# Optimization experiments

Measured on AMD Instinct MI355X. Metric: run time of the kernel, lower is better.

## Reference

```python
import jax, jax.numpy as jnp
import numpy as np

N_HEAD = 8
HEAD_DIM = 32  # 256 / 8
MASK_VALUE = -10000.0

def setup_inputs() -> dict:
    key = jax.random.key(0)
    k1, k2, k3 = jax.random.split(key, 3)
    B, S, D = 8, 2048, 256
    x = jax.random.normal(k1, (B, S, D), dtype=jnp.float32)
    # kaiming_normal fan_in-based std ~ sqrt(2/fan_in)
    w_qkv = jax.random.normal(k2, (3 * D, D), dtype=jnp.float32) * np.sqrt(2.0 / D)
    b_qkv = jnp.zeros((3 * D,), dtype=jnp.float32)
    w_out = jax.random.normal(k3, (D, D), dtype=jnp.float32) * np.sqrt(2.0 / D)
    b_out = jnp.zeros((D,), dtype=jnp.float32)
    return {"x": x, "w_qkv": w_qkv, "b_qkv": b_qkv, "w_out": w_out, "b_out": b_out}

def reference(x, w_qkv, b_qkv, w_out, b_out):
    B, S, D = x.shape
    qkv = x @ w_qkv.T + b_qkv                      # [B,S,3D]
    q, k, v = jnp.split(qkv, 3, axis=-1)           # each [B,S,D]
    def split_heads(t):
        return t.reshape(B, S, N_HEAD, HEAD_DIM).transpose(0, 2, 1, 3)  # [B,H,S,hd]
    q, k, v = split_heads(q), split_heads(k), split_heads(v)
    scores = jnp.einsum('bhqd,bhkd->bhqk', q, k) / jnp.sqrt(jnp.float32(HEAD_DIM))
    causal = jnp.tril(jnp.ones((S, S), dtype=bool))
    scores = jnp.where(causal[None, None], scores, jnp.float32(MASK_VALUE))
    attn = jax.nn.softmax(scores, axis=-1)          # dropout p=0 (eval)
    out = jnp.einsum('bhqk,bhkd->bhqd', attn, v)    # [B,H,S,hd]
    out = out.transpose(0, 2, 1, 3).reshape(B, S, D)  # merge heads
    out = out @ w_out.T + b_out
    return (out, attn)
```

## Files before the change

kernel.cpp:

```cpp
#include <hip/hip_runtime.h>
#include <cmath>

#define NB 8
#define NS 2048
#define ND 256
#define NH 8
#define HD 32
#define NM (NB*NS)
#define QS_LOG2 (0.17677669529663689f * 1.4426950408889634f)
#define OUT_ATTN ((size_t)NM * ND)

typedef __attribute__((ext_vector_type(8))) short bf16x8;
typedef __attribute__((ext_vector_type(4))) float f32x4;

__device__ __forceinline__ ushort f2b(float f) {
  union { float f; uint32_t u; } v; v.f = f;
  const uint32_t r = (v.u + 0x7FFFu + ((v.u >> 16) & 1u)) >> 16;
  return (ushort)r;
}
__device__ __forceinline__ float b2f(ushort u) {
  union { uint32_t u; float f; } v; v.u = ((uint32_t)u) << 16;
  return v.f;
}

__global__ __launch_bounds__(256) void prep_kernel(
    const float* __restrict__ x, const float* __restrict__ wq,
    const float* __restrict__ wo,
    ushort* __restrict__ xh, ushort* __restrict__ xl,
    ushort* __restrict__ wqh, ushort* __restrict__ wql,
    ushort* __restrict__ woh) {
  const int g = blockIdx.x * 256 + threadIdx.x;
  if (g < 1048576) {
    const float4 v = ((const float4*)x)[g];
    ushort4 h, l;
    h.x = f2b(v.x); l.x = f2b(v.x - b2f(h.x));
    h.y = f2b(v.y); l.y = f2b(v.y - b2f(h.y));
    h.z = f2b(v.z); l.z = f2b(v.z - b2f(h.z));
    h.w = f2b(v.w); l.w = f2b(v.w - b2f(h.w));
    ((ushort4*)xh)[g] = h; ((ushort4*)xl)[g] = l;
  } else if (g < 1048576 + 49152) {
    const int t = g - 1048576;
    const float4 v = ((const float4*)wq)[t];
    ushort4 h, l;
    h.x = f2b(v.x); l.x = f2b(v.x - b2f(h.x));
    h.y = f2b(v.y); l.y = f2b(v.y - b2f(h.y));
    h.z = f2b(v.z); l.z = f2b(v.z - b2f(h.z));
    h.w = f2b(v.w); l.w = f2b(v.w - b2f(h.w));
    ((ushort4*)wqh)[t] = h; ((ushort4*)wql)[t] = l;
  } else if (g < 1048576 + 49152 + 16384) {
    const int t = g - (1048576 + 49152);
    const float4 v = ((const float4*)wo)[t];
    ushort4 h;
    h.x = f2b(v.x); h.y = f2b(v.y); h.z = f2b(v.z); h.w = f2b(v.w);
    ((ushort4*)woh)[t] = h;
  }
}

__global__ __launch_bounds__(256) void qkv_kernel(
    const ushort* __restrict__ xh, const ushort* __restrict__ xl,
    const ushort* __restrict__ wqh, const ushort* __restrict__ wql,
    const float* __restrict__ bias,
    ushort* __restrict__ Qb, ushort* __restrict__ Kb, ushort* __restrict__ Vt) {
  __shared__ ushort Bh[128][40];
  __shared__ ushort Bl[128][40];
  const int m0 = blockIdx.x * 64;
  const int n0 = blockIdx.y * 128;
  const int tid  = threadIdx.x;
  const int w = tid >> 6, lane = tid & 63;
  const int a = lane & 15, qd = lane >> 4;
  const int srow = tid & 127, sop = tid >> 7;
  const f32x4 zero4 = {0.f, 0.f, 0.f, 0.f};
  f32x4 acc[8] = {zero4, zero4, zero4, zero4, zero4, zero4, zero4, zero4};

  const size_t arow = (size_t)(m0 + w*16 + a) * ND;
  const ushort* __restrict__ bsrc = (sop ? wql : wqh) + (size_t)(n0 + srow) * ND;

  for (int ks = 0; ks < 8; ++ks) {
    const int kofs = ks * 32;
    const bf16x8 t0 = *(const bf16x8*)&bsrc[kofs + 0];
    const bf16x8 t1 = *(const bf16x8*)&bsrc[kofs + 8];
    const bf16x8 t2 = *(const bf16x8*)&bsrc[kofs + 16];
    const bf16x8 t3 = *(const bf16x8*)&bsrc[kofs + 24];
    const bf16x8 ah = *(const bf16x8*)&xh[arow + kofs + qd*8];
    const bf16x8 al = *(const bf16x8*)&xl[arow + kofs + qd*8];
    __syncthreads();
    ushort (* __restrict__ Bs)[40] = sop ? Bl : Bh;
    *(bf16x8*)&Bs[srow][0]  = t0;
    *(bf16x8*)&Bs[srow][8]  = t1;
    *(bf16x8*)&Bs[srow][16] = t2;
    *(bf16x8*)&Bs[srow][24] = t3;
    __syncthreads();
#pragma unroll
    for (int nt = 0; nt < 8; ++nt) {
      const bf16x8 bhf = *(const bf16x8*)&Bh[nt*16 + a][qd*8];
      const bf16x8 blf = *(const bf16x8*)&Bl[nt*16 + a][qd*8];
      acc[nt] = __builtin_amdgcn_mfma_f32_16x16x32_bf16(al, bhf, acc[nt], 0, 0, 0);
      acc[nt] = __builtin_amdgcn_mfma_f32_16x16x32_bf16(ah, blf, acc[nt], 0, 0, 0);
      acc[nt] = __builtin_amdgcn_mfma_f32_16x16x32_bf16(ah, bhf, acc[nt], 0, 0, 0);
    }
  }

  const int mbase = m0 + w*16 + qd*4;
  const int bb = mbase >> 11, ss = mbase & 2047;
#pragma unroll
  for (int nt = 0; nt < 8; ++nt) {
    const int n = n0 + nt*16 + a;
    const int which = n >> 8;
    const int h = (n >> 5) & 7, e0 = n & 31;
    const float bz = bias[n];
    if (which < 2) {
      const float scl = (which == 0) ? QS_LOG2 : 1.0f;
      ushort* const dst = ((which == 0) ? Qb : Kb) + (size_t)(bb*NH + h) * NS * HD;
#pragma unroll
      for (int r = 0; r < 4; ++r)
        dst[(size_t)(ss + r) * HD + e0] = f2b((acc[nt][r] + bz) * scl);
    } else {
      ushort4 o;
      o.x = f2b(acc[nt][0] + bz);
      o.y = f2b(acc[nt][1] + bz);
      o.z = f2b(acc[nt][2] + bz);
      o.w = f2b(acc[nt][3] + bz);
      *(ushort4*)&Vt[((size_t)(bb*NH + h)*HD + e0) * NS + ss] = o;
    }
  }
}

__global__ __launch_bounds__(256) void denom_kernel(
    const ushort* __restrict__ Qb, const ushort* __restrict__ Kb,
    float* __restrict__ mcbuf) {
  const int bh = blockIdx.x;
  const int qt = (NS / 64 - 1) - blockIdx.y;
  const int q0 = qt * 64;
  const int lane = threadIdx.x & 63;
  const int w    = threadIdx.x >> 6;
  const int a    = lane & 15;
  const int qd   = lane >> 4;
  const ushort* __restrict__ Qh = Qb + (size_t)bh * NS * HD;
  const ushort* __restrict__ Kh = Kb + (size_t)bh * NS * HD;

  const f32x4 zero4 = {0.f, 0.f, 0.f, 0.f};
  const bf16x8 qf = *(const bf16x8*)&Qh[(size_t)(q0 + w*16 + a) * HD + qd*8];

  bf16x8 kf[4], kn[4];
#pragma unroll
  for (int jt = 0; jt < 4; ++jt)
    kf[jt] = *(const bf16x8*)&Kh[(size_t)(jt*16 + a) * HD + qd*8];

  float l_l[4] = {0.f, 0.f, 0.f, 0.f};
  for (int kt = 0; kt <= qt; ++kt) {
    const bool diag = (kt == qt);
    const int lim = diag ? w : 3;
    if (kt < qt) {
      const int k0n = (kt + 1) * 64;
#pragma unroll
      for (int jt = 0; jt < 4; ++jt)
        kn[jt] = *(const bf16x8*)&Kh[(size_t)(k0n + jt*16 + a) * HD + qd*8];
    }
#pragma unroll
    for (int jt = 0; jt < 4; ++jt) {
      if (jt > lim) continue;
      const f32x4 s = __builtin_amdgcn_mfma_f32_16x16x32_bf16(qf, kf[jt], zero4, 0, 0, 0);
      if (diag && jt == w) {
#pragma unroll
        for (int r = 0; r < 4; ++r)
          l_l[r] += (a > qd*4 + r) ? 0.f : exp2f(s[r]);
      } else {
#pragma unroll
        for (int r = 0; r < 4; ++r)
          l_l[r] += exp2f(s[r]);
      }
    }
#pragma unroll
    for (int jt = 0; jt < 4; ++jt) kf[jt] = kn[jt];
  }
#pragma unroll
  for (int r = 0; r < 4; ++r) {
    float c = l_l[r];
#pragma unroll
    for (int off = 1; off < 16; off <<= 1) c += __shfl_xor(c, off);
    if (a == 0)
      mcbuf[(size_t)bh * NS + q0 + w*16 + qd*4 + r] = log2f(c);
  }
}

__global__ __launch_bounds__(256) void attn_kernel(
    const ushort* __restrict__ Qb, const ushort* __restrict__ Kb,
    const ushort* __restrict__ Vt, const float* __restrict__ mcbuf,
    float* __restrict__ attn, ushort* __restrict__ Om) {
  __shared__ float Ps[64][68];
  const int bh = blockIdx.x;
  const int qt = (NS / 64 - 1) - blockIdx.y;
  const int q0 = qt * 64;
  const int lane = threadIdx.x & 63;
  const int w    = threadIdx.x >> 6;
  const int a    = lane & 15;
  const int qd   = lane >> 4;
  const ushort* __restrict__ Qh = Qb + (size_t)bh * NS * HD;
  const ushort* __restrict__ Kh = Kb + (size_t)bh * NS * HD;
  const ushort* __restrict__ Vh = Vt + (size_t)bh * HD * NS;

  const f32x4 zero4 = {0.f, 0.f, 0.f, 0.f};
  const bf16x8 qf = *(const bf16x8*)&Qh[(size_t)(q0 + w*16 + a) * HD + qd*8];
  const float4 mc4 = *(const float4*)&mcbuf[(size_t)bh * NS + q0 + w*16 + qd*4];
  const float mc[4] = {mc4.x, mc4.y, mc4.z, mc4.w};
  float* const attnRow = attn + ((size_t)bh * NS + q0) * NS;

  bf16x8 kf[4], kn[4], vf[4], vn[4];
#pragma unroll
  for (int jt = 0; jt < 4; ++jt)
    kf[jt] = *(const bf16x8*)&Kh[(size_t)(jt*16 + a) * HD + qd*8];
  vf[0] = *(const bf16x8*)&Vh[(size_t)(a)      * NS + qd*8];
  vf[1] = *(const bf16x8*)&Vh[(size_t)(16 + a) * NS + qd*8];
  vf[2] = *(const bf16x8*)&Vh[(size_t)(a)      * NS + 32 + qd*8];
  vf[3] = *(const bf16x8*)&Vh[(size_t)(16 + a) * NS + 32 + qd*8];

  for (int kt = qt + 1; kt < NS / 64; ++kt) {
    const int k0 = kt * 64;
    const float4 z = make_float4(0.f, 0.f, 0.f, 0.f);
#pragma unroll
    for (int i = 0; i < 4; ++i)
      *(float4*)&attnRow[(size_t)(w*16 + i*4 + qd) * NS + k0 + a*4] = z;
  }

  f32x4 oc0 = zero4, oc1 = zero4;

  for (int kt = 0; kt <= qt; ++kt) {
    const int k0 = kt * 64;
    const bool diag = (kt == qt);
    const int lim = diag ? w : 3;

    if (kt < qt) {
      const int k0n = k0 + 64;
#pragma unroll
      for (int jt = 0; jt < 4; ++jt)
        kn[jt] = *(const bf16x8*)&Kh[(size_t)(k0n + jt*16 + a) * HD + qd*8];
      vn[0] = *(const bf16x8*)&Vh[(size_t)(a)      * NS + k0n + qd*8];
      vn[1] = *(const bf16x8*)&Vh[(size_t)(16 + a) * NS + k0n + qd*8];
      vn[2] = *(const bf16x8*)&Vh[(size_t)(a)      * NS + k0n + 32 + qd*8];
      vn[3] = *(const bf16x8*)&Vh[(size_t)(16 + a) * NS + k0n + 32 + qd*8];
    }

#pragma unroll
    for (int jt = 0; jt < 4; ++jt) {
      if (jt > lim) {
#pragma unroll
        for (int r = 0; r < 4; ++r)
          Ps[w*16 + qd*4 + r][jt*16 + a] = 0.f;
        continue;
      }
      const f32x4 s = __builtin_amdgcn_mfma_f32_16x16x32_bf16(qf, kf[jt], zero4, 0, 0, 0);
      if (diag && jt == w) {
#pragma unroll
        for (int r = 0; r < 4; ++r)
          Ps[w*16 + qd*4 + r][jt*16 + a] =
              (a > qd*4 + r) ? 0.f : exp2f(s[r] - mc[r]);
      } else {
#pragma unroll
        for (int r = 0; r < 4; ++r)
          Ps[w*16 + qd*4 + r][jt*16 + a] = exp2f(s[r] - mc[r]);
      }
    }

#pragma unroll
    for (int i = 0; i < 4; ++i) {
      const int row16 = i*4 + qd;
      *(float4*)&attnRow[(size_t)(w*16 + row16) * NS + k0 + a*4] =
          *(const float4*)&Ps[w*16 + row16][a*4];
    }

#pragma unroll
    for (int half = 0; half < 2; ++half) {
      const float4 p0 = *(const float4*)&Ps[w*16 + a][half*32 + qd*8];
      const float4 p1 = *(const float4*)&Ps[w*16 + a][half*32 + qd*8 + 4];
      bf16x8 pa;
      pa[0] = (short)f2b(p0.x); pa[1] = (short)f2b(p0.y);
      pa[2] = (short)f2b(p0.z); pa[3] = (short)f2b(p0.w);
      pa[4] = (short)f2b(p1.x); pa[5] = (short)f2b(p1.y);
      pa[6] = (short)f2b(p1.z); pa[7] = (short)f2b(p1.w);
      oc0 = __builtin_amdgcn_mfma_f32_16x16x32_bf16(pa, half ? vf[2] : vf[0], oc0, 0, 0, 0);
      oc1 = __builtin_amdgcn_mfma_f32_16x16x32_bf16(pa, half ? vf[3] : vf[1], oc1, 0, 0, 0);
    }
#pragma unroll
    for (int jt = 0; jt < 4; ++jt) { kf[jt] = kn[jt]; vf[jt] = vn[jt]; }
  }

  const int bb = bh >> 3, hh = bh & 7;
#pragma unroll
  for (int r = 0; r < 4; ++r) {
    const size_t om = (size_t)(bb * NS + q0 + w*16 + qd*4 + r) * ND + hh*32;
    Om[om + a]      = f2b(oc0[r]);
    Om[om + 16 + a] = f2b(oc1[r]);
  }
}

__global__ __launch_bounds__(256) void proj_kernel(
    const ushort* __restrict__ Om, const ushort* __restrict__ woh,
    const float* __restrict__ bias, float* __restrict__ out) {
  const int m0 = blockIdx.x * 64;
  const int nb = blockIdx.y * 64;
  const int w = threadIdx.x >> 6, lane = threadIdx.x & 63;
  const int a = lane & 15, qd = lane >> 4;
  const f32x4 zero4 = {0.f, 0.f, 0.f, 0.f};
  f32x4 acc[4] = {zero4, zero4, zero4, zero4};
  const size_t arow = (size_t)(m0 + w*16 + a) * ND;
#pragma unroll
  for (int ks = 0; ks < 8; ++ks) {
    const int kofs = ks * 32 + qd * 8;
    const bf16x8 af = *(const bf16x8*)&Om[arow + kofs];
#pragma unroll
    for (int nt = 0; nt < 4; ++nt) {
      const bf16x8 bfg = *(const bf16x8*)&woh[(size_t)(nb + nt*16 + a) * ND + kofs];
      acc[nt] = __builtin_amdgcn_mfma_f32_16x16x32_bf16(af, bfg, acc[nt], 0, 0, 0);
    }
  }
#pragma unroll
  for (int nt = 0; nt < 4; ++nt) {
    const int n = nb + nt*16 + a;
    const float bz = bias[n];
#pragma unroll
    for (int r = 0; r < 4; ++r)
      out[(size_t)(m0 + w*16 + qd*4 + r) * ND + n] = acc[nt][r] + bz;
  }
}

extern "C" void kernel_launch(void* const* d_in, const int* in_sizes, int n_in,
                              void* d_out, int out_size, void* d_ws, size_t ws_size,
                              hipStream_t stream) {
  const float* x     = (const float*)d_in[0];
  const float* w_qkv = (const float*)d_in[1];
  const float* b_qkv = (const float*)d_in[2];
  const float* w_out = (const float*)d_in[3];
  const float* b_out = (const float*)d_in[4];
  float* out  = (float*)d_out;
  float* attn = out + OUT_ATTN;

  ushort* u = (ushort*)d_ws;
  const size_t SZH = (size_t)NB * NH * NS * HD;
  ushort* Qb  = u;  u += SZH;
  ushort* Kb  = u;  u += SZH;
  ushort* Vt  = u;  u += SZH;
  ushort* Om  = u;  u += SZH;
  ushort* xh  = u;  u += SZH;
  ushort* xl  = u;  u += SZH;
  ushort* wqh = u;  u += (size_t)768 * ND;
  ushort* wql = u;  u += (size_t)768 * ND;
  ushort* woh = u;  u += (size_t)ND * ND;
  float* mcbuf = (float*)u;

  prep_kernel<<<4352, 256, 0, stream>>>(x, w_qkv, w_out, xh, xl, wqh, wql, woh);
  qkv_kernel<<<dim3(NM / 64, 768 / 128), 256, 0, stream>>>(xh, xl, wqh, wql, b_qkv, Qb, Kb, Vt);
  denom_kernel<<<dim3(NB * NH, NS / 64), 256, 0, stream>>>(Qb, Kb, mcbuf);
  attn_kernel<<<dim3(NB * NH, NS / 64), 256, 0, stream>>>(Qb, Kb, Vt, mcbuf, attn, Om);
  proj_kernel<<<dim3(NM / 64, ND / 64), 256, 0, stream>>>(Om, woh, b_out, out);
}
```

Baseline: 347.9 us.

## Fuse softmax denominator pass into attention kernel and use nontemporal attn stores

Removes the separate denom_kernel launch and its mcbuf round-trip by computing the row-sum of exp2 scores inside attn_kernel as a first pass over K. The zero-fill of the masked upper triangle is interleaved with that first pass so the stores overlap with the compute. All attention-matrix stores now use nontemporal stores to avoid polluting the cache. Each block now does two passes over K, so per-block latency grows, but a launch and global traffic for the denominators are eliminated.

```diff
diff --git a/kernel.cpp b/kernel.cpp
--- a/kernel.cpp
+++ b/kernel.cpp
@@ -125,68 +125,10 @@
   }
 }
 
-__global__ __launch_bounds__(256) void denom_kernel(
-    const ushort* __restrict__ Qb, const ushort* __restrict__ Kb,
-    float* __restrict__ mcbuf) {
-  const int bh = blockIdx.x;
-  const int qt = (NS / 64 - 1) - blockIdx.y;
-  const int q0 = qt * 64;
-  const int lane = threadIdx.x & 63;
-  const int w    = threadIdx.x >> 6;
-  const int a    = lane & 15;
-  const int qd   = lane >> 4;
-  const ushort* __restrict__ Qh = Qb + (size_t)bh * NS * HD;
-  const ushort* __restrict__ Kh = Kb + (size_t)bh * NS * HD;
-
-  const f32x4 zero4 = {0.f, 0.f, 0.f, 0.f};
-  const bf16x8 qf = *(const bf16x8*)&Qh[(size_t)(q0 + w*16 + a) * HD + qd*8];
-
-  bf16x8 kf[4], kn[4];
-#pragma unroll
-  for (int jt = 0; jt < 4; ++jt)
-    kf[jt] = *(const bf16x8*)&Kh[(size_t)(jt*16 + a) * HD + qd*8];
-
-  float l_l[4] = {0.f, 0.f, 0.f, 0.f};
-  for (int kt = 0; kt <= qt; ++kt) {
-    const bool diag = (kt == qt);
-    const int lim = diag ? w : 3;
-    if (kt < qt) {
-      const int k0n = (kt + 1) * 64;
-#pragma unroll
-      for (int jt = 0; jt < 4; ++jt)
-        kn[jt] = *(const bf16x8*)&Kh[(size_t)(k0n + jt*16 + a) * HD + qd*8];
-    }
-#pragma unroll
-    for (int jt = 0; jt < 4; ++jt) {
-      if (jt > lim) continue;
-      const f32x4 s = __builtin_amdgcn_mfma_f32_16x16x32_bf16(qf, kf[jt], zero4, 0, 0, 0);
-      if (diag && jt == w) {
-#pragma unroll
-        for (int r = 0; r < 4; ++r)
-          l_l[r] += (a > qd*4 + r) ? 0.f : exp2f(s[r]);
-      } else {
-#pragma unroll
-        for (int r = 0; r < 4; ++r)
-          l_l[r] += exp2f(s[r]);
-      }
-    }
-#pragma unroll
-    for (int jt = 0; jt < 4; ++jt) kf[jt] = kn[jt];
-  }
-#pragma unroll
-  for (int r = 0; r < 4; ++r) {
-    float c = l_l[r];
-#pragma unroll
-    for (int off = 1; off < 16; off <<= 1) c += __shfl_xor(c, off);
-    if (a == 0)
-      mcbuf[(size_t)bh * NS + q0 + w*16 + qd*4 + r] = log2f(c);
-  }
-}
-
 __global__ __launch_bounds__(256) void attn_kernel(
     const ushort* __restrict__ Qb, const ushort* __restrict__ Kb,
-    const ushort* __restrict__ Vt, const float* __restrict__ mcbuf,
-    float* __restrict__ attn, ushort* __restrict__ Om) {
+    const ushort* __restrict__ Vt, float* __restrict__ attn,
+    ushort* __restrict__ Om) {
   __shared__ float Ps[64][68];
   const int bh = blockIdx.x;
   const int qt = (NS / 64 - 1) - blockIdx.y;
@@ -201,11 +143,50 @@
 
   const f32x4 zero4 = {0.f, 0.f, 0.f, 0.f};
   const bf16x8 qf = *(const bf16x8*)&Qh[(size_t)(q0 + w*16 + a) * HD + qd*8];
-  const float4 mc4 = *(const float4*)&mcbuf[(size_t)bh * NS + q0 + w*16 + qd*4];
-  const float mc[4] = {mc4.x, mc4.y, mc4.z, mc4.w};
   float* const attnRow = attn + ((size_t)bh * NS + q0) * NS;
 
   bf16x8 kf[4], kn[4], vf[4], vn[4];
+#pragma unroll
+  for (int jt = 0; jt < 4; ++jt)
+    kf[jt] = *(const bf16x8*)&Kh[(size_t)(jt*16 + a) * HD + qd*8];
+
+  float l_l[4] = {0.f, 0.f, 0.f, 0.f};
+  int zt = qt + 1;
+  for (int kt = 0; kt <= qt; ++kt) {
+    const bool diag = (kt == qt);
+    const int lim = diag ? w : 3;
+    if (kt < qt) {
+      const int k0n = (kt + 1) * 64;
+#pragma unroll
+      for (int jt = 0; jt < 4; ++jt)
+        kn[jt] = *(const bf16x8*)&Kh[(size_t)(k0n + jt*16 + a) * HD + qd*8];
+    }
+    if (zt < NS / 64) {
+      const int z0 = zt * 64;
+#pragma unroll
+      for (int i = 0; i < 4; ++i)
+        __builtin_nontemporal_store(zero4,
+            (f32x4*)&attnRow[(size_t)(w*16 + i*4 + qd) * NS + z0 + a*4]);
+      ++zt;
+    }
+#pragma unroll
+    for (int jt = 0; jt < 4; ++jt) {
+      if (jt > lim) continue;
+      const f32x4 s = __builtin_amdgcn_mfma_f32_16x16x32_bf16(qf, kf[jt], zero4, 0, 0, 0);
+      if (diag && jt == w) {
+#pragma unroll
+        for (int r = 0; r < 4; ++r)
+          l_l[r] += (a > qd*4 + r) ? 0.f : exp2f(s[r]);
+      } else {
+#pragma unroll
+        for (int r = 0; r < 4; ++r)
+          l_l[r] += exp2f(s[r]);
+      }
+    }
+#pragma unroll
+    for (int jt = 0; jt < 4; ++jt) kf[jt] = kn[jt];
+  }
+
 #pragma unroll
   for (int jt = 0; jt < 4; ++jt)
     kf[jt] = *(const bf16x8*)&Kh[(size_t)(jt*16 + a) * HD + qd*8];
@@ -214,12 +195,21 @@
   vf[2] = *(const bf16x8*)&Vh[(size_t)(a)      * NS + 32 + qd*8];
   vf[3] = *(const bf16x8*)&Vh[(size_t)(16 + a) * NS + 32 + qd*8];
 
-  for (int kt = qt + 1; kt < NS / 64; ++kt) {
-    const int k0 = kt * 64;
-    const float4 z = make_float4(0.f, 0.f, 0.f, 0.f);
+  for (; zt < NS / 64; ++zt) {
+    const int z0 = zt * 64;
 #pragma unroll
     for (int i = 0; i < 4; ++i)
-      *(float4*)&attnRow[(size_t)(w*16 + i*4 + qd) * NS + k0 + a*4] = z;
+      __builtin_nontemporal_store(zero4,
+          (f32x4*)&attnRow[(size_t)(w*16 + i*4 + qd) * NS + z0 + a*4]);
+  }
+
+  float mc[4];
+#pragma unroll
+  for (int r = 0; r < 4; ++r) {
+    float c = l_l[r];
+#pragma unroll
+    for (int off = 1; off < 16; off <<= 1) c += __shfl_xor(c, off);
+    mc[r] = log2f(c);
   }
 
   f32x4 oc0 = zero4, oc1 = zero4;
@@ -264,8 +254,9 @@
 #pragma unroll
     for (int i = 0; i < 4; ++i) {
       const int row16 = i*4 + qd;
-      *(float4*)&attnRow[(size_t)(w*16 + row16) * NS + k0 + a*4] =
-          *(const float4*)&Ps[w*16 + row16][a*4];
+      const f32x4 pv = *(const f32x4*)&Ps[w*16 + row16][a*4];
+      __builtin_nontemporal_store(pv,
+          (f32x4*)&attnRow[(size_t)(w*16 + row16) * NS + k0 + a*4]);
     }
 
 #pragma unroll
@@ -345,11 +336,9 @@
   ushort* wqh = u;  u += (size_t)768 * ND;
   ushort* wql = u;  u += (size_t)768 * ND;
   ushort* woh = u;  u += (size_t)ND * ND;
-  float* mcbuf = (float*)u;
 
   prep_kernel<<<4352, 256, 0, stream>>>(x, w_qkv, w_out, xh, xl, wqh, wql, woh);
   qkv_kernel<<<dim3(NM / 64, 768 / 128), 256, 0, stream>>>(xh, xl, wqh, wql, b_qkv, Qb, Kb, Vt);
-  denom_kernel<<<dim3(NB * NH, NS / 64), 256, 0, stream>>>(Qb, Kb, mcbuf);
-  attn_kernel<<<dim3(NB * NH, NS / 64), 256, 0, stream>>>(Qb, Kb, Vt, mcbuf, attn, Om);
+  attn_kernel<<<dim3(NB * NH, NS / 64), 256, 0, stream>>>(Qb, Kb, Vt, attn, Om);
   proj_kernel<<<dim3(NM / 64, ND / 64), 256, 0, stream>>>(Om, woh, b_out, out);
 }
```

Result: faster. 314.0 us (-9.7%).
